# Optimization experiments

Measured on AMD Instinct MI355X. Metric: run time of the kernel, lower is better.

## Reference

```python
import jax, jax.numpy as jnp
import numpy as np

B, T, D = 1024, 512, 64   # batch, seq_len, input_dim
H, L, OUT = 8, 3, 1       # hidden (mid_dim), num_layers, output_dim


def setup_inputs() -> dict:
    key = jax.random.key(0)
    ks = jax.random.split(key, 18)
    s = 1.0 / np.sqrt(H)  # torch LSTM default init scale
    u = lambda k, shape: jax.random.uniform(k, shape, jnp.float32, -s, s)
    return {
        "input_seq": jax.random.normal(ks[0], (B, T, D), jnp.float32),
        "h0": jax.random.normal(ks[1], (L, B, H), jnp.float32),
        "c0": jax.random.normal(ks[2], (L, B, H), jnp.float32),
        # encoder LSTM params (layer0 input dim differs)
        "enc_Wih0": u(ks[3], (4 * H, D)),
        "enc_Wih_rest": u(ks[4], (L - 1, 4 * H, H)),
        "enc_Whh": u(ks[5], (L, 4 * H, H)),
        "enc_bih": u(ks[6], (L, 4 * H)),
        "enc_bhh": u(ks[7], (L, 4 * H)),
        # decoder LSTM params
        "dec_Wih0": u(ks[8], (4 * H, D)),
        "dec_Wih_rest": u(ks[9], (L - 1, 4 * H, H)),
        "dec_Whh": u(ks[10], (L, 4 * H, H)),
        "dec_bih": u(ks[11], (L, 4 * H)),
        "dec_bhh": u(ks[12], (L, 4 * H)),
        # decoder output projection
        "lin_W": u(ks[13], (OUT, H)),
        "lin_b": u(ks[14], (OUT,)),
    }


def _cell(x, h, c, Wih, Whh, b):
    # one LSTM cell step, torch gate order: i, f, g, o
    gates = x @ Wih.T + h @ Whh.T + b  # [B, 4H]
    i, f, g, o = jnp.split(gates, 4, axis=-1)
    c2 = jax.nn.sigmoid(f) * c + jax.nn.sigmoid(i) * jnp.tanh(g)
    h2 = jax.nn.sigmoid(o) * jnp.tanh(c2)
    return h2, c2


def _stack_step(h, c, x_t, Wih0, Wih_rest, Whh, bih, bhh):
    # one timestep through all L layers; h, c: [L, B, H]
    hs, cs = [], []
    inp = x_t
    for l in range(L):
        Wih = Wih0 if l == 0 else Wih_rest[l - 1]
        h_l, c_l = _cell(inp, h[l], c[l], Wih, Whh[l], bih[l] + bhh[l])
        hs.append(h_l)
        cs.append(c_l)
        inp = h_l
    return jnp.stack(hs), jnp.stack(cs)


def reference(input_seq, h0, c0, enc_Wih0, enc_Wih_rest, enc_Whh, enc_bih, enc_bhh,
              dec_Wih0, dec_Wih_rest, dec_Whh, dec_bih, dec_bhh, lin_W, lin_b):
    x_tbd = jnp.transpose(input_seq, (1, 0, 2))  # [T, B, D] for scan

    # Encoder: full-sequence 3-layer LSTM, keep final (h, c)
    def enc_step(carry, x_t):
        h, c = carry
        h2, c2 = _stack_step(h, c, x_t, enc_Wih0, enc_Wih_rest, enc_Whh, enc_bih, enc_bhh)
        return (h2, c2), None

    (h, c), _ = jax.lax.scan(enc_step, (h0, c0), x_tbd)

    # Decoder: one LSTM step per timestep, fed the input at that step
    def dec_step(carry, x_t):
        h, c = carry
        h2, c2 = _stack_step(h, c, x_t, dec_Wih0, dec_Wih_rest, dec_Whh, dec_bih, dec_bhh)
        return (h2, c2), None

    (h, c), _ = jax.lax.scan(dec_step, (h, c), x_tbd)

    # original returns outputs[:, -1, :] = linear applied to last decoder output
    pred_last = h[-1] @ lin_W.T + lin_b  # [B, OUT]
    return pred_last
```

## Files before the change

kernel.cpp:

```cpp
#include <hip/hip_runtime.h>

#define TT 512
#define DD 64
#define BB 1024
#define PF 8
#define HH 8
#define WBLK 32
#define NWIN (TT / WBLK)

__device__ __forceinline__ float fexp2(float x){ return __builtin_amdgcn_exp2f(x); }
__device__ __forceinline__ float frcp (float x){ return __builtin_amdgcn_rcpf(x); }

template<int C>
__device__ __forceinline__ float dppf(float x){
  return __int_as_float(__builtin_amdgcn_update_dpp(0, __float_as_int(x), C, 0xF, 0xF, true));
}
template<int C>
__device__ __forceinline__ int dppi(int x){
  return __builtin_amdgcn_update_dpp(0, x, C, 0xF, 0xF, true);
}

__device__ __forceinline__ float swz16(float x){
  return __int_as_float(__builtin_amdgcn_ds_swizzle(__float_as_int(x), 0x401F));
}

template<int N> struct IC { static constexpr int v = N; };

__global__ __launch_bounds__(256) void fused_kernel(
    const float* __restrict__ x,
    const float* __restrict__ h0,    const float* __restrict__ c0,
    const float* __restrict__ eWih0, const float* __restrict__ eWihR, const float* __restrict__ eWhh,
    const float* __restrict__ eBih,  const float* __restrict__ eBhh,
    const float* __restrict__ dWih0, const float* __restrict__ dWihR, const float* __restrict__ dWhh,
    const float* __restrict__ dBih,  const float* __restrict__ dBhh,
    const float* __restrict__ linW,  const float* __restrict__ linB,
    float* __restrict__ out)
{
  extern __shared__ __align__(16) float smem[];
  float* Pbuf = smem;
  float* xst  = smem + 2 * WBLK * 4 * 32;

  const int tid  = threadIdx.x;
  const int wv   = tid >> 6;
  const int lane = tid & 63;
  const bool prod = (wv >= 2);

  const int idx = tid & 31;
  const int v   = idx >> 2;
  const int g   = idx & 3;
  const int b   = v & 3;
  const bool rB = (v >= 4);
  const int erow = tid >> 5;
  const int e    = blockIdx.x * 4 + erow;

  const bool is_tanh = (g == 2);
  const float ns_act = is_tanh ? -2.885390082f : -1.44269504f;
  const float a_act  = is_tanh ? 2.0f : 1.0f;
  const float b_act  = is_tanh ? -1.0f : 0.0f;

  const int qidx = (tid >> 2) & 3;
  const int p4 = dppi<0x124>(qidx);
  const int d  = __builtin_amdgcn_readfirstlane((p4 - qidx) & 3);

  float H[3], cs[3], sd[3];
  float bd1 = 0.f, bd2 = 0.f;
  float WS[3][8], WBr[2][8], Bss[2];

  if (!prod) {
#pragma unroll
    for (int l = 0; l < 3; ++l) {
      H[l]  = h0[((size_t)l * BB + e) * HH + v];
      cs[l] = c0[((size_t)l * BB + e) * HH + v];
    }
  }

  const int rsel = lane >> 4;
  const int m    = lane & 15;
  const int r_even = (m >> 2) * 8 + (m & 3);
  const int r_odd  = r_even + 4;
  const int p0 = (wv - 2) * 2;
  float Wa[64], Wb[64];
  float bA = 0.f, bB = 0.f;

  auto bcast = [&](float hn, float* A, float* Bv) {
    float Hsw = swz16(hn);
    float Lo = rB ? Hsw : hn;
    float Hi = rB ? hn : Hsw;
    A[0]  = Lo; A[1]  = dppf<0x124>(Lo); A[2]  = dppf<0x128>(Lo); A[3]  = dppf<0x12C>(Lo);
    Bv[0] = Hi; Bv[1] = dppf<0x124>(Hi); Bv[2] = dppf<0x128>(Hi); Bv[3] = dppf<0x12C>(Hi);
  };

  auto load_phase = [&](const float* WihR, const float* Whh,
                        const float* Bih, const float* Bhh) {
#pragma unroll
    for (int l = 0; l < 3; ++l) {
      const int r0 = l * 32 + g * 8 + v;
#pragma unroll
      for (int k = 0; k < 4; ++k) {
        const int col = (b + d * k) & 3;
        WS[l][k]     = Whh[r0 * 8 + col];
        WS[l][4 + k] = Whh[r0 * 8 + 4 + col];
      }
    }
#pragma unroll
    for (int l = 0; l < 2; ++l) {
      const int r0 = l * 32 + g * 8 + v;
#pragma unroll
      for (int k = 0; k < 4; ++k) {
        const int col = (b + d * k) & 3;
        WBr[l][k]     = WihR[r0 * 8 + col];
        WBr[l][4 + k] = WihR[r0 * 8 + 4 + col];
      }
      Bss[l] = Bih[(l + 1) * 32 + g * 8 + v] + Bhh[(l + 1) * 32 + g * 8 + v];
    }
#pragma unroll
    for (int l = 0; l < 3; ++l) {
      float A[4], Bv[4];
      bcast(H[l], A, Bv);
      float acc = l ? Bss[l - 1] : 0.f;
#pragma unroll
      for (int k = 0; k < 4; ++k) {
        acc = fmaf(WS[l][k],     A[k],  acc);
        acc = fmaf(WS[l][4 + k], Bv[k], acc);
      }
      sd[l] = acc;
    }
  };

  auto lstep = [&](auto LC, float in) -> float {
    constexpr int l = decltype(LC)::v;
    float pre = in + sd[l];
    float ex  = fexp2(ns_act * pre);
    float rc  = frcp(1.f + ex);
    float act = fmaf(a_act, rc, b_act);
    float Gi = dppf<0x00>(act);
    float Gf = dppf<0x55>(act);
    float Gg = dppf<0xAA>(act);
    float Go = dppf<0xFF>(act);
    float cn = fmaf(Gf, cs[l], Gi * Gg);
    cs[l] = cn;
    float tx = fexp2(-2.885390082f * cn);
    float tr = frcp(1.f + tx);
    float th = fmaf(2.f, tr, -1.f);
    float hn = Go * th;
    H[l] = hn;
    float A[4], Bv[4];
    bcast(hn, A, Bv);
    float accS;
    if constexpr (l > 0) accS = Bss[l - 1]; else accS = 0.f;
#pragma unroll
    for (int k = 0; k < 4; ++k) {
      accS = fmaf(WS[l][k],     A[k],  accS);
      accS = fmaf(WS[l][4 + k], Bv[k], accS);
    }
    sd[l] = accS;
    float accB = 0.f;
    if constexpr (l < 2) {
#pragma unroll
      for (int k = 0; k < 4; ++k) {
        accB = fmaf(WBr[l][k],     A[k],  accB);
        accB = fmaf(WBr[l][4 + k], Bv[k], accB);
      }
    }
    return accB;
  };

  auto lstep3 = [&](float in0, float in1, float in2, float& nb1, float& nb2) {
    float pre0 = in0 + sd[0];
    float pre1 = in1 + sd[1];
    float pre2 = in2 + sd[2];
    float ex0 = fexp2(ns_act * pre0);
    float ex1 = fexp2(ns_act * pre1);
    float ex2 = fexp2(ns_act * pre2);
    float rc0 = frcp(1.f + ex0);
    float rc1 = frcp(1.f + ex1);
    float rc2 = frcp(1.f + ex2);
    float ac0 = fmaf(a_act, rc0, b_act);
    float ac1 = fmaf(a_act, rc1, b_act);
    float ac2 = fmaf(a_act, rc2, b_act);
    float Gi0 = dppf<0x00>(ac0), Gi1 = dppf<0x00>(ac1), Gi2 = dppf<0x00>(ac2);
    float Gf0 = dppf<0x55>(ac0), Gf1 = dppf<0x55>(ac1), Gf2 = dppf<0x55>(ac2);
    float Gg0 = dppf<0xAA>(ac0), Gg1 = dppf<0xAA>(ac1), Gg2 = dppf<0xAA>(ac2);
    float Go0 = dppf<0xFF>(ac0), Go1 = dppf<0xFF>(ac1), Go2 = dppf<0xFF>(ac2);
    float cn0 = fmaf(Gf0, cs[0], Gi0 * Gg0);
    float cn1 = fmaf(Gf1, cs[1], Gi1 * Gg1);
    float cn2 = fmaf(Gf2, cs[2], Gi2 * Gg2);
    cs[0] = cn0; cs[1] = cn1; cs[2] = cn2;
    float tx0 = fexp2(-2.885390082f * cn0);
    float tx1 = fexp2(-2.885390082f * cn1);
    float tx2 = fexp2(-2.885390082f * cn2);
    float tr0 = frcp(1.f + tx0);
    float tr1 = frcp(1.f + tx1);
    float tr2 = frcp(1.f + tx2);
    float th0 = fmaf(2.f, tr0, -1.f);
    float th1 = fmaf(2.f, tr1, -1.f);
    float th2 = fmaf(2.f, tr2, -1.f);
    float hn0 = Go0 * th0;
    float hn1 = Go1 * th1;
    float hn2 = Go2 * th2;
    H[0] = hn0; H[1] = hn1; H[2] = hn2;
    float sw0 = swz16(hn0);
    float sw1 = swz16(hn1);
    float sw2 = swz16(hn2);
    float Lo0 = rB ? sw0 : hn0, Hi0 = rB ? hn0 : sw0;
    float Lo1 = rB ? sw1 : hn1, Hi1 = rB ? hn1 : sw1;
    float Lo2 = rB ? sw2 : hn2, Hi2 = rB ? hn2 : sw2;
    float A0[4], B0[4], A1[4], B1[4], A2[4], B2[4];
    A0[0] = Lo0; A0[1] = dppf<0x124>(Lo0); A0[2] = dppf<0x128>(Lo0); A0[3] = dppf<0x12C>(Lo0);
    B0[0] = Hi0; B0[1] = dppf<0x124>(Hi0); B0[2] = dppf<0x128>(Hi0); B0[3] = dppf<0x12C>(Hi0);
    A1[0] = Lo1; A1[1] = dppf<0x124>(Lo1); A1[2] = dppf<0x128>(Lo1); A1[3] = dppf<0x12C>(Lo1);
    B1[0] = Hi1; B1[1] = dppf<0x124>(Hi1); B1[2] = dppf<0x128>(Hi1); B1[3] = dppf<0x12C>(Hi1);
    A2[0] = Lo2; A2[1] = dppf<0x124>(Lo2); A2[2] = dppf<0x128>(Lo2); A2[3] = dppf<0x12C>(Lo2);
    B2[0] = Hi2; B2[1] = dppf<0x124>(Hi2); B2[2] = dppf<0x128>(Hi2); B2[3] = dppf<0x12C>(Hi2);
    float s0 = 0.f, s1 = Bss[0], s2 = Bss[1];
    float u0 = 0.f, u1 = 0.f;
#pragma unroll
    for (int k = 0; k < 4; ++k) {
      s0 = fmaf(WS[0][k],     A0[k], s0);
      s0 = fmaf(WS[0][4 + k], B0[k], s0);
      s1 = fmaf(WS[1][k],     A1[k], s1);
      s1 = fmaf(WS[1][4 + k], B1[k], s1);
      s2 = fmaf(WS[2][k],     A2[k], s2);
      s2 = fmaf(WS[2][4 + k], B2[k], s2);
      u0 = fmaf(WBr[0][k],     A0[k], u0);
      u0 = fmaf(WBr[0][4 + k], B0[k], u0);
      u1 = fmaf(WBr[1][k],     A1[k], u1);
      u1 = fmaf(WBr[1][4 + k], B1[k], u1);
    }
    sd[0] = s0; sd[1] = s1; sd[2] = s2;
    nb1 = u0; nb2 = u1;
  };

  const int pos_c = (g * 4 + b) * 2 + (v >> 2);

  auto consume = [&](int w) {
    const float* Pw = Pbuf + ((w & 1) * WBLK * 4 * 32) + erow * 32 + pos_c;
    float pf[PF];
#pragma unroll
    for (int k = 0; k < PF; ++k) pf[k] = Pw[k * 128];
    if (w == 0) {
#pragma unroll
      for (int k = 0; k < PF; ++k) {
        float cur = pf[k];
        pf[k] = Pw[(PF + k) * 128];
        float n1 = lstep(IC<0>{}, cur);
        float n2 = 0.f;
        if (k >= 1) n2 = lstep(IC<1>{}, bd1);
        if (k >= 2) (void)lstep(IC<2>{}, bd2);
        bd1 = n1; bd2 = n2;
      }
#pragma unroll 1
      for (int gi = 1; gi < 3; ++gi) {
#pragma unroll
        for (int j = 0; j < PF; ++j) {
          float cur = pf[j];
          pf[j] = Pw[((gi + 1) * PF + j) * 128];
          float n1, n2;
          lstep3(cur, bd1, bd2, n1, n2);
          bd1 = n1; bd2 = n2;
        }
      }
    } else {
#pragma unroll 1
      for (int gi = 0; gi < 3; ++gi) {
#pragma unroll
        for (int j = 0; j < PF; ++j) {
          float cur = pf[j];
          pf[j] = Pw[((gi + 1) * PF + j) * 128];
          float n1, n2;
          lstep3(cur, bd1, bd2, n1, n2);
          bd1 = n1; bd2 = n2;
        }
      }
    }
#pragma unroll
    for (int j = 0; j < PF; ++j) {
      float cur = pf[j];
      float n1, n2;
      lstep3(cur, bd1, bd2, n1, n2);
      bd1 = n1; bd2 = n2;
    }
  };

  auto produce = [&](int w, int buf) {
#pragma unroll 1
    for (int es = 0; es < 2; ++es) {
      const int p  = p0 + es;
      const float* xg = x + ((size_t)(blockIdx.x * 4 + p) * TT + w * WBLK) * 64;
      float* xp = xst + p * (WBLK * 64);
      float4 sv[8];
#pragma unroll
      for (int i = 0; i < 8; ++i) sv[i] = *(const float4*)(xg + i * 256 + lane * 4);
#pragma unroll
      for (int i = 0; i < 8; ++i) *(float4*)(xp + i * 256 + lane * 4) = sv[i];
#pragma unroll 1
      for (int ci = 0; ci < 8; ++ci) {
        const int rib = ci * 4 + rsel;
        const float* xr = xp + rib * 64;
        float a0A = bA, a1A = 0.f, a2A = 0.f, a3A = 0.f;
        float a0B = bB, a1B = 0.f, a2B = 0.f, a3B = 0.f;
#pragma unroll
        for (int kc = 0; kc < 16; ++kc) {
          float4 xv = *(const float4*)(xr + kc * 4);
          a0A = fmaf(Wa[kc*4+0], xv.x, a0A);
          a1A = fmaf(Wa[kc*4+1], xv.y, a1A);
          a2A = fmaf(Wa[kc*4+2], xv.z, a2A);
          a3A = fmaf(Wa[kc*4+3], xv.w, a3A);
          a0B = fmaf(Wb[kc*4+0], xv.x, a0B);
          a1B = fmaf(Wb[kc*4+1], xv.y, a1B);
          a2B = fmaf(Wb[kc*4+2], xv.z, a2B);
          a3B = fmaf(Wb[kc*4+3], xv.w, a3B);
        }
        float2 res;
        res.x = (a0A + a1A) + (a2A + a3A);
        res.y = (a0B + a1B) + (a2B + a3B);
        *(float2*)(Pbuf + ((size_t)(buf * WBLK + rib) * 4 + p) * 32 + 2 * m) = res;
      }
    }
  };

#pragma unroll 1
  for (int ph = 0; ph < 2; ++ph) {
    if (prod) {
      const float* W  = ph ? dWih0 : eWih0;
      const float* Bi = ph ? dBih  : eBih;
      const float* Bh = ph ? dBhh  : eBhh;
      bA = Bi[r_even] + Bh[r_even];
      bB = Bi[r_odd]  + Bh[r_odd];
#pragma unroll
      for (int k = 0; k < 16; ++k) {
        float4 wq = *(const float4*)(W + r_even * 64 + k * 4);
        Wa[k*4+0] = wq.x; Wa[k*4+1] = wq.y; Wa[k*4+2] = wq.z; Wa[k*4+3] = wq.w;
      }
#pragma unroll
      for (int k = 0; k < 16; ++k) {
        float4 wq = *(const float4*)(W + r_odd * 64 + k * 4);
        Wb[k*4+0] = wq.x; Wb[k*4+1] = wq.y; Wb[k*4+2] = wq.z; Wb[k*4+3] = wq.w;
      }
      produce(0, 0);
    } else {
      if (ph == 0) load_phase(eWihR, eWhh, eBih, eBhh);
      else         load_phase(dWihR, dWhh, dBih, dBhh);
    }
    __syncthreads();

#pragma unroll 1
    for (int w = 0; w < NWIN; ++w) {
      if (prod) {
        if (w < NWIN - 1) produce(w + 1, (w + 1) & 1);
      } else {
        consume(w);
      }
      __syncthreads();
    }

    if (!prod) {
      float dd = lstep(IC<1>{}, bd1);
      (void)lstep(IC<2>{}, bd2);
      (void)lstep(IC<2>{}, dd);
    }
  }

  if (!prod) {
    float lwA[4], lwB[4];
#pragma unroll
    for (int k = 0; k < 4; ++k) {
      const int col = (b + d * k) & 3;
      lwA[k] = linW[col];
      lwB[k] = linW[4 + col];
    }
    float A[4], Bv[4];
    bcast(H[2], A, Bv);
    float pred = linB[0];
#pragma unroll
    for (int k = 0; k < 4; ++k) {
      pred = fmaf(lwA[k], A[k],  pred);
      pred = fmaf(lwB[k], Bv[k], pred);
    }
    if (idx == 0) out[e] = pred;
  }
}

extern "C" void kernel_launch(void* const* d_in, const int* in_sizes, int n_in,
                              void* d_out, int out_size, void* d_ws, size_t ws_size,
                              hipStream_t stream) {
  const float* x     = (const float*)d_in[0];
  const float* h0    = (const float*)d_in[1];
  const float* c0    = (const float*)d_in[2];
  const float* eWih0 = (const float*)d_in[3];
  const float* eWihR = (const float*)d_in[4];
  const float* eWhh  = (const float*)d_in[5];
  const float* eBih  = (const float*)d_in[6];
  const float* eBhh  = (const float*)d_in[7];
  const float* dWih0 = (const float*)d_in[8];
  const float* dWihR = (const float*)d_in[9];
  const float* dWhh  = (const float*)d_in[10];
  const float* dBih  = (const float*)d_in[11];
  const float* dBhh  = (const float*)d_in[12];
  const float* linW  = (const float*)d_in[13];
  const float* linB  = (const float*)d_in[14];
  float* out = (float*)d_out;

  fused_kernel<<<BB / 4, 256, 98304, stream>>>(
      x, h0, c0, eWih0, eWihR, eWhh, eBih, eBhh,
      dWih0, dWihR, dWhh, dBih, dBhh, linW, linB, out);
}
```

Baseline: 521.0 us.

## Stage layer-0 input projections in global workspace with cross-phase producer lookahead

Producers now write the layer-0 input projections for both encoder and decoder into a global workspace buffer instead of a double-buffered LDS ring. The producer runs two windows ahead across the encoder/decoder boundary, so the decoder's weights and first windows are ready before the encoder finishes. The x staging tile is padded to avoid LDS bank conflicts. A simple fallback kernel runs when the workspace is too small. This removes the per-phase pipeline drain and refill, but the consumer now reads projections from global memory (L2) instead of LDS, which adds latency on the recurrent critical path and extra HBM traffic.

```diff
diff --git a/kernel.cpp b/kernel.cpp
--- a/kernel.cpp
+++ b/kernel.cpp
@@ -6,7 +6,7 @@
 #define PF 8
 #define HH 8
 #define WBLK 32
-#define NWIN (TT / WBLK)
+#define XPAD 68
 
 __device__ __forceinline__ float fexp2(float x){ return __builtin_amdgcn_exp2f(x); }
 __device__ __forceinline__ float frcp (float x){ return __builtin_amdgcn_rcpf(x); }
@@ -34,11 +34,10 @@
     const float* __restrict__ dWih0, const float* __restrict__ dWihR, const float* __restrict__ dWhh,
     const float* __restrict__ dBih,  const float* __restrict__ dBhh,
     const float* __restrict__ linW,  const float* __restrict__ linB,
+    float* __restrict__ P,
     float* __restrict__ out)
 {
   extern __shared__ __align__(16) float smem[];
-  float* Pbuf = smem;
-  float* xst  = smem + 2 * WBLK * 4 * 32;
 
   const int tid  = threadIdx.x;
   const int wv   = tid >> 6;
@@ -64,6 +63,7 @@
 
   float H[3], cs[3], sd[3];
   float bd1 = 0.f, bd2 = 0.f;
+  float pf[PF];
   float WS[3][8], WBr[2][8], Bss[2];
 
   if (!prod) {
@@ -79,8 +79,67 @@
   const int r_even = (m >> 2) * 8 + (m & 3);
   const int r_odd  = r_even + 4;
   const int p0 = (wv - 2) * 2;
+  float* xp = smem + (wv & 1) * (WBLK * XPAD);
   float Wa[64], Wb[64];
   float bA = 0.f, bB = 0.f;
+  int curph = 0;
+
+  auto loadW = [&](int ph) {
+    const float* W  = ph ? dWih0 : eWih0;
+    const float* Bi = ph ? dBih  : eBih;
+    const float* Bh = ph ? dBhh  : eBhh;
+    bA = Bi[r_even] + Bh[r_even];
+    bB = Bi[r_odd]  + Bh[r_odd];
+#pragma unroll
+    for (int k = 0; k < 16; ++k) {
+      float4 wq = *(const float4*)(W + r_even * 64 + k * 4);
+      Wa[k*4+0] = wq.x; Wa[k*4+1] = wq.y; Wa[k*4+2] = wq.z; Wa[k*4+3] = wq.w;
+    }
+#pragma unroll
+    for (int k = 0; k < 16; ++k) {
+      float4 wq = *(const float4*)(W + r_odd * 64 + k * 4);
+      Wb[k*4+0] = wq.x; Wb[k*4+1] = wq.y; Wb[k*4+2] = wq.z; Wb[k*4+3] = wq.w;
+    }
+  };
+
+  auto produce = [&](int ph, int w) {
+    if (ph != curph) { loadW(ph); curph = ph; }
+#pragma unroll 1
+    for (int es = 0; es < 2; ++es) {
+      const int p  = p0 + es;
+      const int eE = blockIdx.x * 4 + p;
+      const float* xg = x + ((size_t)eE * TT + w * WBLK) * 64;
+      float4 sv[8];
+#pragma unroll
+      for (int i = 0; i < 8; ++i) sv[i] = *(const float4*)(xg + i * 256 + lane * 4);
+#pragma unroll
+      for (int i = 0; i < 8; ++i)
+        *(float4*)(xp + (i * 4 + (lane >> 4)) * XPAD + 4 * (lane & 15)) = sv[i];
+#pragma unroll 1
+      for (int ci = 0; ci < 8; ++ci) {
+        const int rib = ci * 4 + rsel;
+        const float* xr = xp + rib * XPAD;
+        float a0A = bA, a1A = 0.f, a2A = 0.f, a3A = 0.f;
+        float a0B = bB, a1B = 0.f, a2B = 0.f, a3B = 0.f;
+#pragma unroll
+        for (int kc = 0; kc < 16; ++kc) {
+          float4 xv = *(const float4*)(xr + kc * 4);
+          a0A = fmaf(Wa[kc*4+0], xv.x, a0A);
+          a1A = fmaf(Wa[kc*4+1], xv.y, a1A);
+          a2A = fmaf(Wa[kc*4+2], xv.z, a2A);
+          a3A = fmaf(Wa[kc*4+3], xv.w, a3A);
+          a0B = fmaf(Wb[kc*4+0], xv.x, a0B);
+          a1B = fmaf(Wb[kc*4+1], xv.y, a1B);
+          a2B = fmaf(Wb[kc*4+2], xv.z, a2B);
+          a3B = fmaf(Wb[kc*4+3], xv.w, a3B);
+        }
+        float2 res;
+        res.x = (a0A + a1A) + (a2A + a3A);
+        res.y = (a0B + a1B) + (a2B + a3B);
+        *(float2*)(P + ((size_t)((ph << 10) + eE) * TT + (w * WBLK + rib)) * 32 + 2 * m) = res;
+      }
+    }
+  };
 
   auto bcast = [&](float hn, float* A, float* Bv) {
     float Hsw = swz16(hn);
@@ -233,132 +292,88 @@
 
   const int pos_c = (g * 4 + b) * 2 + (v >> 2);
 
-  auto consume = [&](int w) {
-    const float* Pw = Pbuf + ((w & 1) * WBLK * 4 * 32) + erow * 32 + pos_c;
-    float pf[PF];
-#pragma unroll
-    for (int k = 0; k < PF; ++k) pf[k] = Pw[k * 128];
-    if (w == 0) {
-#pragma unroll
-      for (int k = 0; k < PF; ++k) {
-        float cur = pf[k];
-        pf[k] = Pw[(PF + k) * 128];
-        float n1 = lstep(IC<0>{}, cur);
-        float n2 = 0.f;
-        if (k >= 1) n2 = lstep(IC<1>{}, bd1);
-        if (k >= 2) (void)lstep(IC<2>{}, bd2);
-        bd1 = n1; bd2 = n2;
-      }
+  if (prod) {
+    loadW(0);
+    produce(0, 0);
+    produce(0, 1);
+  }
+  __syncthreads();
+
 #pragma unroll 1
-      for (int gi = 1; gi < 3; ++gi) {
+  for (int win = 0; win < 32; ++win) {
+    if (prod) {
+      const int item = win + 2;
+      if (item < 32) produce(item >> 4, item & 15);
+    } else {
+      const int ph = win >> 4;
+      const int w  = win & 15;
+      const float* Pb = P + ((size_t)((ph << 10) + e) * TT) * 32 + pos_c;
+      if (w == 0) {
+        if (ph == 0) load_phase(eWihR, eWhh, eBih, eBhh);
+        else         load_phase(dWihR, dWhh, dBih, dBhh);
+#pragma unroll
+        for (int k = 0; k < PF; ++k) pf[k] = Pb[k * 32];
+#pragma unroll
+        for (int k = 0; k < PF; ++k) {
+          float cur = pf[k];
+          pf[k] = Pb[(k + PF) * 32];
+          float n1 = lstep(IC<0>{}, cur);
+          float n2 = 0.f;
+          if (k >= 1) n2 = lstep(IC<1>{}, bd1);
+          if (k >= 2) (void)lstep(IC<2>{}, bd2);
+          bd1 = n1; bd2 = n2;
+        }
+#pragma unroll 1
+        for (int gi = 1; gi < 4; ++gi) {
+          const float* Pq = Pb + (size_t)((gi + 1) * PF) * 32;
+#pragma unroll
+          for (int j = 0; j < PF; ++j) {
+            float cur = pf[j];
+            pf[j] = Pq[j * 32];
+            float n1, n2;
+            lstep3(cur, bd1, bd2, n1, n2);
+            bd1 = n1; bd2 = n2;
+          }
+        }
+      } else if (w < 15) {
+#pragma unroll 1
+        for (int gi = 0; gi < 4; ++gi) {
+          const float* Pq = Pb + (size_t)(w * WBLK + gi * PF + PF) * 32;
+#pragma unroll
+          for (int j = 0; j < PF; ++j) {
+            float cur = pf[j];
+            pf[j] = Pq[j * 32];
+            float n1, n2;
+            lstep3(cur, bd1, bd2, n1, n2);
+            bd1 = n1; bd2 = n2;
+          }
+        }
+      } else {
+#pragma unroll 1
+        for (int gi = 0; gi < 3; ++gi) {
+          const float* Pq = Pb + (size_t)(480 + gi * PF + PF) * 32;
+#pragma unroll
+          for (int j = 0; j < PF; ++j) {
+            float cur = pf[j];
+            pf[j] = Pq[j * 32];
+            float n1, n2;
+            lstep3(cur, bd1, bd2, n1, n2);
+            bd1 = n1; bd2 = n2;
+          }
+        }
 #pragma unroll
         for (int j = 0; j < PF; ++j) {
           float cur = pf[j];
-          pf[j] = Pw[((gi + 1) * PF + j) * 128];
           float n1, n2;
           lstep3(cur, bd1, bd2, n1, n2);
           bd1 = n1; bd2 = n2;
         }
-      }
-    } else {
-#pragma unroll 1
-      for (int gi = 0; gi < 3; ++gi) {
-#pragma unroll
-        for (int j = 0; j < PF; ++j) {
-          float cur = pf[j];
-          pf[j] = Pw[((gi + 1) * PF + j) * 128];
-          float n1, n2;
-          lstep3(cur, bd1, bd2, n1, n2);
-          bd1 = n1; bd2 = n2;
-        }
-      }
-    }
-#pragma unroll
-    for (int j = 0; j < PF; ++j) {
-      float cur = pf[j];
-      float n1, n2;
-      lstep3(cur, bd1, bd2, n1, n2);
-      bd1 = n1; bd2 = n2;
-    }
-  };
-
-  auto produce = [&](int w, int buf) {
-#pragma unroll 1
-    for (int es = 0; es < 2; ++es) {
-      const int p  = p0 + es;
-      const float* xg = x + ((size_t)(blockIdx.x * 4 + p) * TT + w * WBLK) * 64;
-      float* xp = xst + p * (WBLK * 64);
-      float4 sv[8];
-#pragma unroll
-      for (int i = 0; i < 8; ++i) sv[i] = *(const float4*)(xg + i * 256 + lane * 4);
-#pragma unroll
-      for (int i = 0; i < 8; ++i) *(float4*)(xp + i * 256 + lane * 4) = sv[i];
-#pragma unroll 1
-      for (int ci = 0; ci < 8; ++ci) {
-        const int rib = ci * 4 + rsel;
-        const float* xr = xp + rib * 64;
-        float a0A = bA, a1A = 0.f, a2A = 0.f, a3A = 0.f;
-        float a0B = bB, a1B = 0.f, a2B = 0.f, a3B = 0.f;
-#pragma unroll
-        for (int kc = 0; kc < 16; ++kc) {
-          float4 xv = *(const float4*)(xr + kc * 4);
-          a0A = fmaf(Wa[kc*4+0], xv.x, a0A);
-          a1A = fmaf(Wa[kc*4+1], xv.y, a1A);
-          a2A = fmaf(Wa[kc*4+2], xv.z, a2A);
-          a3A = fmaf(Wa[kc*4+3], xv.w, a3A);
-          a0B = fmaf(Wb[kc*4+0], xv.x, a0B);
-          a1B = fmaf(Wb[kc*4+1], xv.y, a1B);
-          a2B = fmaf(Wb[kc*4+2], xv.z, a2B);
-          a3B = fmaf(Wb[kc*4+3], xv.w, a3B);
-        }
-        float2 res;
-        res.x = (a0A + a1A) + (a2A + a3A);
-        res.y = (a0B + a1B) + (a2B + a3B);
-        *(float2*)(Pbuf + ((size_t)(buf * WBLK + rib) * 4 + p) * 32 + 2 * m) = res;
-      }
-    }
-  };
-
-#pragma unroll 1
-  for (int ph = 0; ph < 2; ++ph) {
-    if (prod) {
-      const float* W  = ph ? dWih0 : eWih0;
-      const float* Bi = ph ? dBih  : eBih;
-      const float* Bh = ph ? dBhh  : eBhh;
-      bA = Bi[r_even] + Bh[r_even];
-      bB = Bi[r_odd]  + Bh[r_odd];
-#pragma unroll
-      for (int k = 0; k < 16; ++k) {
-        float4 wq = *(const float4*)(W + r_even * 64 + k * 4);
-        Wa[k*4+0] = wq.x; Wa[k*4+1] = wq.y; Wa[k*4+2] = wq.z; Wa[k*4+3] = wq.w;
-      }
-#pragma unroll
-      for (int k = 0; k < 16; ++k) {
-        float4 wq = *(const float4*)(W + r_odd * 64 + k * 4);
-        Wb[k*4+0] = wq.x; Wb[k*4+1] = wq.y; Wb[k*4+2] = wq.z; Wb[k*4+3] = wq.w;
-      }
-      produce(0, 0);
-    } else {
-      if (ph == 0) load_phase(eWihR, eWhh, eBih, eBhh);
-      else         load_phase(dWihR, dWhh, dBih, dBhh);
+        float dd = lstep(IC<1>{}, bd1);
+        (void)lstep(IC<2>{}, bd2);
+        (void)lstep(IC<2>{}, dd);
+      }
     }
     __syncthreads();
-
-#pragma unroll 1
-    for (int w = 0; w < NWIN; ++w) {
-      if (prod) {
-        if (w < NWIN - 1) produce(w + 1, (w + 1) & 1);
-      } else {
-        consume(w);
-      }
-      __syncthreads();
-    }
-
-    if (!prod) {
-      float dd = lstep(IC<1>{}, bd1);
-      (void)lstep(IC<2>{}, bd2);
-      (void)lstep(IC<2>{}, dd);
-    }
   }
 
   if (!prod) {
@@ -379,6 +394,97 @@
     }
     if (idx == 0) out[e] = pred;
   }
+}
+
+__global__ __launch_bounds__(64) void seq2seq_fallback(
+    const float* __restrict__ x, const float* __restrict__ h0, const float* __restrict__ c0,
+    const float* __restrict__ eWih0, const float* __restrict__ eWihR, const float* __restrict__ eWhh,
+    const float* __restrict__ eBih,  const float* __restrict__ eBhh,
+    const float* __restrict__ dWih0, const float* __restrict__ dWihR, const float* __restrict__ dWhh,
+    const float* __restrict__ dBih,  const float* __restrict__ dBhh,
+    const float* __restrict__ linW,  const float* __restrict__ linB, float* __restrict__ out)
+{
+  const int tid = threadIdx.x;
+  const int g   = tid & 31;
+  const int grp = tid & 32;
+  const int jj  = g & 7;
+  const int e   = blockIdx.x * 2 + (tid >> 5);
+  const bool is_tanh = ((g >> 3) == 2);
+  const float s_act = is_tanh ? 2.885390082f : 1.44269504f;
+  const float a_act = is_tanh ? 2.0f : 1.0f;
+  const float b_act = is_tanh ? -1.0f : 0.0f;
+  float hrep[3][8]; float cc[3];
+#pragma unroll
+  for (int l = 0; l < 3; ++l) {
+#pragma unroll
+    for (int k = 0; k < 8; ++k) hrep[l][k] = h0[((size_t)l * BB + e) * HH + k];
+    cc[l] = c0[((size_t)l * BB + e) * HH + jj];
+  }
+  for (int p = 0; p < 2; ++p) {
+    const float* Wih0 = p ? dWih0 : eWih0;  const float* WihR = p ? dWihR : eWihR;
+    const float* Whh  = p ? dWhh  : eWhh;   const float* Bih  = p ? dBih  : eBih;
+    const float* Bhh  = p ? dBhh  : eBhh;
+    float Wx[64];
+#pragma unroll
+    for (int k = 0; k < 64; k += 4) {
+      float4 w = *(const float4*)(Wih0 + g * 64 + k);
+      Wx[k] = w.x; Wx[k+1] = w.y; Wx[k+2] = w.z; Wx[k+3] = w.w;
+    }
+    float Wh[3][8], Wi[2][8], bias[3];
+#pragma unroll
+    for (int l = 0; l < 3; ++l) {
+#pragma unroll
+      for (int k = 0; k < 8; ++k) Wh[l][k] = Whh[(l*32+g)*8+k];
+      bias[l] = Bih[l*32+g] + Bhh[l*32+g];
+    }
+#pragma unroll
+    for (int l = 0; l < 2; ++l)
+#pragma unroll
+      for (int k = 0; k < 8; ++k) Wi[l][k] = WihR[(l*32+g)*8+k];
+    const float* xrow = x + (size_t)e * TT * DD;
+    for (int t = 0; t < TT; ++t) {
+      float4 acc = make_float4(bias[0], 0.f, 0.f, 0.f);
+#pragma unroll
+      for (int kc = 0; kc < 16; ++kc) {
+        float4 xv = *(const float4*)(xrow + kc * 4);
+        acc.x = fmaf(Wx[kc*4+0], xv.x, acc.x); acc.y = fmaf(Wx[kc*4+1], xv.y, acc.y);
+        acc.z = fmaf(Wx[kc*4+2], xv.z, acc.z); acc.w = fmaf(Wx[kc*4+3], xv.w, acc.w);
+      }
+      float pre = (acc.x + acc.y) + (acc.z + acc.w);
+      { float r0=0.f,r1=0.f;
+#pragma unroll
+        for (int k = 0; k < 8; k += 2) { r0=fmaf(Wh[0][k],hrep[0][k],r0); r1=fmaf(Wh[0][k+1],hrep[0][k+1],r1); }
+        pre += r0 + r1; }
+#pragma unroll
+      for (int l = 0; l < 3; ++l) {
+        if (l > 0) {
+          float r0 = bias[l], r1 = 0.f;
+#pragma unroll
+          for (int k = 0; k < 8; k += 2) {
+            r0=fmaf(Wi[l-1][k],hrep[l-1][k],r0); r1=fmaf(Wi[l-1][k+1],hrep[l-1][k+1],r1);
+            r0=fmaf(Wh[l][k],hrep[l][k],r0);     r1=fmaf(Wh[l][k+1],hrep[l][k+1],r1);
+          }
+          pre = r0 + r1;
+        }
+        float act = fmaf(a_act, frcp(1.0f + fexp2(-s_act * pre)), b_act);
+        float iv = __shfl(act, grp + jj);
+        float fv = __shfl(act, grp + 8 + jj);
+        float gv = __shfl(act, grp + 16 + jj);
+        float ov = __shfl(act, grp + 24 + jj);
+        float cn = fmaf(fv, cc[l], iv * gv);
+        cc[l] = cn;
+        float th = fmaf(2.0f, frcp(1.0f + fexp2(-2.885390082f * cn)), -1.0f);
+        float hn = ov * th;
+#pragma unroll
+        for (int k = 0; k < 8; ++k) hrep[l][k] = __shfl(hn, grp + k);
+      }
+      xrow += DD;
+    }
+  }
+  float pred = linB[0];
+#pragma unroll
+  for (int k = 0; k < 8; ++k) pred = fmaf(linW[k], hrep[2][k], pred);
+  if (g == 0) out[e] = pred;
 }
 
 extern "C" void kernel_launch(void* const* d_in, const int* in_sizes, int n_in,
@@ -401,7 +507,14 @@
   const float* linB  = (const float*)d_in[14];
   float* out = (float*)d_out;
 
-  fused_kernel<<<BB / 4, 256, 98304, stream>>>(
-      x, h0, c0, eWih0, eWihR, eWhh, eBih, eBhh,
-      dWih0, dWihR, dWhh, dBih, dBhh, linW, linB, out);
+  const size_t P_BYTES = (size_t)2 * BB * TT * 32 * sizeof(float);
+  if (ws_size >= P_BYTES) {
+    float* P = (float*)d_ws;
+    fused_kernel<<<BB / 4, 256, 98304, stream>>>(
+        x, h0, c0, eWih0, eWihR, eWhh, eBih, eBhh,
+        dWih0, dWihR, dWhh, dBih, dBhh, linW, linB, P, out);
+  } else {
+    seq2seq_fallback<<<BB / 2, 64, 0, stream>>>(x, h0, c0, eWih0, eWihR, eWhh, eBih, eBhh,
+                                                dWih0, dWihR, dWhh, dBih, dBhh, linW, linB, out);
+  }
 }
```

New measurement: 1.091 ms. 109% more time.
